# Kernel tuning notes

Hardware: AMD Instinct MI355X
Metric: run time of the kernel (lower is better)

Reference implementation:

```python
import jax, jax.numpy as jnp
import numpy as np

N_CLASSES = 2  # FS-MOL binary labels


def setup_inputs() -> dict:
    key = jax.random.key(0)
    k1, k2, k3 = jax.random.split(key, 3)
    Ns, Nq, d = 512, 16384, 512
    support_features = jax.random.normal(k1, (Ns, d), dtype=jnp.float32)
    support_labels = jax.random.randint(k2, (Ns,), 0, N_CLASSES, dtype=jnp.int64)
    query_features = jax.random.normal(k3, (Nq, d), dtype=jnp.float32)
    return {
        "support_features": support_features,
        "support_labels": support_labels,
        "query_features": query_features,
    }


def _cov(x):
    # rowvar=False covariance of [N, d] -> [d, d], matching _estimate_cov
    xc = x - jnp.mean(x, axis=0, keepdims=True)
    return (xc.T @ xc) / (x.shape[0] - 1)


def reference(support_features, support_labels, query_features):
    d = support_features.shape[1]
    dt = support_features.dtype
    task_cov = _cov(support_features)          # [d, d]
    reg = jnp.asarray(0.1, dt) * jnp.eye(d, dtype=dt)

    def per_class(c):
        mask = (support_labels == c).astype(dt)            # [Ns]
        n = mask.sum()                                      # scalar count
        mean = (mask[:, None] * support_features).sum(0) / n
        xc = (support_features - mean) * mask[:, None]      # zero out other classes
        cov_c = (xc.T @ xc) / (n - 1.0)
        lam = jnp.minimum(n / (n + 1.0), jnp.asarray(0.1, dt))
        prec = jnp.linalg.inv(lam * cov_c + (1.0 - lam) * task_cov + reg)
        return mean, prec

    means, precs = jax.vmap(per_class)(jnp.arange(N_CLASSES))  # [C,d], [C,d,d]

    # Mahalanobis: diff[c,q,:] = mean_c - query_q  (matches repeated_class_means - repeated_target)
    diff = means[:, None, :] - query_features[None, :, :]      # [C, Nq, d]
    h = jnp.einsum('cqd,cde->cqe', diff, precs)                # [C, Nq, d]
    logits = -(h * diff).sum(-1).T                             # [Nq, C]
    return logits
```

## Files before the change

### kernel.cpp

```cpp
#include <hip/hip_runtime.h>

#define NS 512
#define DF 512
#define NQ 16384

#define WS_MEAN0 0
#define WS_MEAN1 512
#define WS_MEANA 1024
#define WS_CNT   1536
#define WS_V0    2048
#define WS_V1    2560
#define WS_KC    3072
#define WS_M     4096
#define WS_PB    (WS_M + 2*DF*DF)
#define WS_QB    (WS_PB + DF*DF)
#define WS_GP    WS_QB

typedef __attribute__((ext_vector_type(8))) short short8;
typedef __attribute__((ext_vector_type(4))) float floatx4;

__device__ __forceinline__ unsigned short f2bf(float f) {
    unsigned u = __float_as_uint(f);
    unsigned r = (u + 0x7fffu + ((u >> 16) & 1u)) >> 16;
    return (unsigned short)r;
}

__device__ __forceinline__ float readlane_f(float v, int lane) {
    return __uint_as_float(__builtin_amdgcn_readlane(__float_as_uint(v), lane));
}

__device__ __forceinline__ void load_lds16(const void* g, void* l) {
    __builtin_amdgcn_global_load_lds(
        (const __attribute__((address_space(1))) unsigned int*)g,
        (__attribute__((address_space(3))) unsigned int*)l, 16, 0, 0);
}

__global__ __launch_bounds__(512) void k_stats(const float* __restrict__ S,
                                               const int* __restrict__ lab,
                                               float* __restrict__ ws) {
    __shared__ int lb[NS];
    __shared__ float r0[8][64], r1[8][64];
    __shared__ int rc[8];
    int tid = threadIdx.x;
    for (int l = tid; l < NS; l += 512) lb[l] = lab[l];
    __syncthreads();
    int dl = tid & 63, ch = tid >> 6;
    int dd = blockIdx.x * 64 + dl;
    float s0 = 0.f, s1 = 0.f;
    int n1 = 0;
    for (int n = ch * 64; n < ch * 64 + 64; ++n) {
        float v = S[n * DF + dd];
        if (lb[n]) { s1 += v; n1++; } else { s0 += v; }
    }
    r0[ch][dl] = s0; r1[ch][dl] = s1;
    if (dl == 0) rc[ch] = n1;
    __syncthreads();
    if (ch == 0) {
        float t0 = 0.f, t1 = 0.f; int n1t = 0;
#pragma unroll
        for (int x = 0; x < 8; ++x) { t0 += r0[x][dl]; t1 += r1[x][dl]; n1t += rc[x]; }
        float fn1 = (float)n1t, fn0 = (float)(NS - n1t);
        ws[WS_MEAN0 + dd] = t0 / fn0;
        ws[WS_MEAN1 + dd] = t1 / fn1;
        ws[WS_MEANA + dd] = (t0 + t1) / (float)NS;
        if (blockIdx.x == 0 && dl == 0) {
            ws[WS_CNT] = fn0; ws[WS_CNT + 1] = fn1;
            ws[WS_KC] = 0.f; ws[WS_KC + 1] = 0.f;
        }
    }
}

__global__ __launch_bounds__(256) void k_gram_part(const float* __restrict__ S,
                                                   const int* __restrict__ lab,
                                                   float* __restrict__ ws) {
    __shared__ float SA[16 * 65];
    __shared__ float SB[16 * 65];
    __shared__ int lb[16];
    int tx = threadIdx.x, ty = threadIdx.y;
    int tid = ty * 16 + tx;
    int i0 = blockIdx.x * 64, j0 = blockIdx.y * 64;
    int z = blockIdx.z;
    float a0[4][4] = {{0.f}}, a1[4][4] = {{0.f}};
    for (int nc = z * 64; nc < z * 64 + 64; nc += 16) {
#pragma unroll
        for (int l = 0; l < 4; ++l) {
            int idx = tid + 256 * l;
            int nn = idx >> 6, col = idx & 63;
            SA[nn * 65 + col] = S[(nc + nn) * DF + i0 + col];
            SB[nn * 65 + col] = S[(nc + nn) * DF + j0 + col];
        }
        if (tid < 16) lb[tid] = lab[nc + tid];
        __syncthreads();
#pragma unroll
        for (int kk = 0; kk < 16; ++kk) {
            float av[4], bv[4];
#pragma unroll
            for (int r = 0; r < 4; ++r) av[r] = SA[kk * 65 + ty * 4 + r];
#pragma unroll
            for (int s = 0; s < 4; ++s) bv[s] = SB[kk * 65 + tx * 4 + s];
            if (lb[kk]) {
#pragma unroll
                for (int r = 0; r < 4; ++r)
#pragma unroll
                    for (int s = 0; s < 4; ++s) a1[r][s] += av[r] * bv[s];
            } else {
#pragma unroll
                for (int r = 0; r < 4; ++r)
#pragma unroll
                    for (int s = 0; s < 4; ++s) a0[r][s] += av[r] * bv[s];
            }
        }
        __syncthreads();
    }
    float* Gp = ws + WS_GP;
#pragma unroll
    for (int r = 0; r < 4; ++r) {
        int i = i0 + ty * 4 + r;
#pragma unroll
        for (int s = 0; s < 4; ++s) {
            int j = j0 + tx * 4 + s;
            Gp[((z * 2 + 0) * DF + i) * DF + j] = a0[r][s];
            Gp[((z * 2 + 1) * DF + i) * DF + j] = a1[r][s];
        }
    }
}

__global__ __launch_bounds__(256) void k_asm(float* __restrict__ ws) {
    const float* Gp = ws + WS_GP;
    int e = blockIdx.x * 256 + threadIdx.x;
    int i = e >> 9, j = e & 511;
    float g0 = 0.f, g1 = 0.f;
#pragma unroll
    for (int ch = 0; ch < 8; ++ch) {
        g0 += Gp[((ch * 2 + 0) * DF + i) * DF + j];
        g1 += Gp[((ch * 2 + 1) * DF + i) * DF + j];
    }
    float n0 = ws[WS_CNT], n1 = ws[WS_CNT + 1];
    float lam0 = fminf(n0 / (n0 + 1.f), 0.1f);
    float lam1 = fminf(n1 / (n1 + 1.f), 0.1f);
    float m0i = ws[WS_MEAN0 + i], m1i = ws[WS_MEAN1 + i], mai = ws[WS_MEANA + i];
    float m0j = ws[WS_MEAN0 + j], m1j = ws[WS_MEAN1 + j], maj = ws[WS_MEANA + j];
    float task = (g0 + g1 - (float)NS * mai * maj) / (float)(NS - 1);
    float cov0 = (g0 - n0 * m0i * m0j) / (n0 - 1.f);
    float cov1 = (g1 - n1 * m1i * m1j) / (n1 - 1.f);
    float dg = (i == j) ? 0.1f : 0.f;
    ws[WS_M + i * DF + j] = lam0 * cov0 + (1.f - lam0) * task + dg;
    ws[WS_M + DF * DF + i * DF + j] = lam1 * cov1 + (1.f - lam1) * task + dg;
}

__global__ __launch_bounds__(256) void k_step(float* __restrict__ ws, int k, int wbf) {
    int c = blockIdx.y;
    int jh = blockIdx.z;
    int ti = blockIdx.x >> 3, tj = blockIdx.x & 7;
    float* Mb = ws + WS_M + c * DF * DF;
    float* Akk = Mb + (k * 64) * DF + k * 64;
    unsigned short* pb = (unsigned short*)(ws + WS_PB) + (size_t)c * DF * DF;
    __shared__ float T[64 * 65];
    __shared__ float LV[64 * 65];
    __shared__ float LU[64 * 33];
    __shared__ float D1[64 * 33];
    __shared__ float rbuf[2][4][64];
    int tid = threadIdx.x;
    int jl = tid & 63, w = tid >> 6;
    bool isdiag = (ti == k) && (tj == k);
    bool isrow = (ti == k) && (tj != k);
    bool iscol = (tj == k) && (ti != k);

#pragma unroll
    for (int m = 0; m < 16; ++m) {
        int idx = tid + 256 * m;
        int i = idx >> 6, j = idx & 63;
        T[i * 65 + j] = Akk[i * DF + j];
    }
    if (ti != k) {
        const float* src = Mb + (ti * 64) * DF + k * 64;
#pragma unroll
        for (int m = 0; m < 16; ++m) {
            int idx = tid + 256 * m;
            int i = idx >> 6, j = idx & 63;
            LV[i * 65 + j] = src[i * DF + j];
        }
    }
    if (tj != k) {
        const float* src = Mb + (k * 64) * DF + tj * 64 + jh * 32;
#pragma unroll
        for (int m = 0; m < 8; ++m) {
            int idx = tid + 256 * m;
            int i = idx >> 5, j = idx & 31;
            LU[i * 33 + j] = src[i * DF + j];
        }
    }
    __syncthreads();

    float Tr[16];
#pragma unroll
    for (int m = 0; m < 16; ++m) Tr[m] = T[(w * 16 + m) * 65 + jl];
#pragma unroll
    for (int r = 0; r < 16; ++r) {
        const int q0 = r * 4;
        const int par = r & 1;
        if (w == (q0 >> 4)) {
            const int mb = q0 & 15;
            rbuf[par][0][jl] = Tr[mb + 0];
            rbuf[par][1][jl] = Tr[mb + 1];
            rbuf[par][2][jl] = Tr[mb + 2];
            rbuf[par][3][jl] = Tr[mb + 3];
        }
        __syncthreads();
        float B[4][4];
#pragma unroll
        for (int a = 0; a < 4; ++a)
#pragma unroll
            for (int b = 0; b < 4; ++b) B[a][b] = rbuf[par][a][q0 + b];
#pragma unroll
        for (int p = 0; p < 4; ++p) {
            float piv = 1.0f / B[p][p];
#pragma unroll
            for (int j = 0; j < 4; ++j) if (j != p) B[p][j] *= piv;
#pragma unroll
            for (int i = 0; i < 4; ++i) if (i != p) {
                float f = B[i][p];
#pragma unroll
                for (int j = 0; j < 4; ++j) if (j != p) B[i][j] -= f * B[p][j];
                B[i][p] = -f * piv;
            }
            B[p][p] = piv;
        }
        float r0v = rbuf[par][0][jl], r1v = rbuf[par][1][jl];
        float r2v = rbuf[par][2][jl], r3v = rbuf[par][3][jl];
        float nr[4];
#pragma unroll
        for (int a = 0; a < 4; ++a)
            nr[a] = B[a][0] * r0v + B[a][1] * r1v + B[a][2] * r2v + B[a][3] * r3v;
        bool colin = ((jl >> 2) == r);
        int bsel = jl & 3;
        float Bc[4];
#pragma unroll
        for (int a = 0; a < 4; ++a)
            Bc[a] = bsel == 0 ? B[a][0]
                  : (bsel == 1 ? B[a][1] : (bsel == 2 ? B[a][2] : B[a][3]));
#pragma unroll
        for (int m = 0; m < 16; ++m) {
            float cv0 = readlane_f(Tr[m], q0 + 0);
            float cv1 = readlane_f(Tr[m], q0 + 1);
            float cv2 = readlane_f(Tr[m], q0 + 2);
            float cv3 = readlane_f(Tr[m], q0 + 3);
            float g = Tr[m] - (cv0 * nr[0] + cv1 * nr[1] + cv2 * nr[2] + cv3 * nr[3]);
            bool rowin = (((w * 16 + m) >> 2) == r);
            float gcol = -(cv0 * Bc[0] + cv1 * Bc[1] + cv2 * Bc[2] + cv3 * Bc[3]);
            if (rowin) g = nr[m & 3];
            if (colin) g = rowin ? Bc[m & 3] : gcol;
            Tr[m] = g;
        }
    }
#pragma unroll
    for (int m = 0; m < 16; ++m) T[(w * 16 + m) * 65 + jl] = Tr[m];
    __syncthreads();

    int tx8 = tid & 7, ty32 = tid >> 3;
    int cb0 = jh * 32;
    if (isdiag) {
#pragma unroll
        for (int m = 0; m < 8; ++m) {
            int idx = tid + 256 * m;
            int i = idx >> 5, j = idx & 31;
            float v = T[i * 65 + cb0 + j];
            Akk[i * DF + cb0 + j] = v;
            if (wbf) pb[(size_t)(k * 64 + i) * DF + k * 64 + cb0 + j] = f2bf(v);
        }
    } else if (isrow) {
        float acc[2][4] = {{0.f}};
        for (int kk = 0; kk < 64; ++kk) {
            float av[2], bv[4];
#pragma unroll
            for (int r = 0; r < 2; ++r) av[r] = T[(ty32 * 2 + r) * 65 + kk];
#pragma unroll
            for (int s = 0; s < 4; ++s) bv[s] = LU[kk * 33 + tx8 * 4 + s];
#pragma unroll
            for (int r = 0; r < 2; ++r)
#pragma unroll
                for (int s = 0; s < 4; ++s) acc[r][s] += av[r] * bv[s];
        }
        float* dst = Mb + (k * 64) * DF + tj * 64 + cb0;
#pragma unroll
        for (int r = 0; r < 2; ++r)
#pragma unroll
            for (int s = 0; s < 4; ++s) {
                float v = acc[r][s];
                dst[(ty32 * 2 + r) * DF + tx8 * 4 + s] = v;
                if (wbf) pb[(size_t)(k * 64 + ty32 * 2 + r) * DF + tj * 64 + cb0 + tx8 * 4 + s] = f2bf(v);
            }
    } else if (iscol) {
        float acc[2][4] = {{0.f}};
        for (int kk = 0; kk < 64; ++kk) {
            float av[2], bv[4];
#pragma unroll
            for (int r = 0; r < 2; ++r) av[r] = LV[(ty32 * 2 + r) * 65 + kk];
#pragma unroll
            for (int s = 0; s < 4; ++s) bv[s] = T[kk * 65 + cb0 + tx8 * 4 + s];
#pragma unroll
            for (int r = 0; r < 2; ++r)
#pragma unroll
                for (int s = 0; s < 4; ++s) acc[r][s] += av[r] * bv[s];
        }
        float* dst = Mb + (ti * 64) * DF + k * 64 + cb0;
#pragma unroll
        for (int r = 0; r < 2; ++r)
#pragma unroll
            for (int s = 0; s < 4; ++s) {
                float v = -acc[r][s];
                dst[(ty32 * 2 + r) * DF + tx8 * 4 + s] = v;
                if (wbf) pb[(size_t)(ti * 64 + ty32 * 2 + r) * DF + k * 64 + cb0 + tx8 * 4 + s] = f2bf(v);
            }
    } else {
        float a1[2][4] = {{0.f}};
        for (int kk = 0; kk < 64; ++kk) {
            float av[2], bv[4];
#pragma unroll
            for (int r = 0; r < 2; ++r) av[r] = T[(ty32 * 2 + r) * 65 + kk];
#pragma unroll
            for (int s = 0; s < 4; ++s) bv[s] = LU[kk * 33 + tx8 * 4 + s];
#pragma unroll
            for (int r = 0; r < 2; ++r)
#pragma unroll
                for (int s = 0; s < 4; ++s) a1[r][s] += av[r] * bv[s];
        }
        __syncthreads();
#pragma unroll
        for (int r = 0; r < 2; ++r)
#pragma unroll
            for (int s = 0; s < 4; ++s) D1[(ty32 * 2 + r) * 33 + tx8 * 4 + s] = a1[r][s];
        __syncthreads();
        float a2[2][4] = {{0.f}};
        for (int kk = 0; kk < 64; ++kk) {
            float av[2], bv[4];
#pragma unroll
            for (int r = 0; r < 2; ++r) av[r] = LV[(ty32 * 2 + r) * 65 + kk];
#pragma unroll
            for (int s = 0; s < 4; ++s) bv[s] = D1[kk * 33 + tx8 * 4 + s];
#pragma unroll
            for (int r = 0; r < 2; ++r)
#pragma unroll
                for (int s = 0; s < 4; ++s) a2[r][s] += av[r] * bv[s];
        }
        float* dst = Mb + (ti * 64) * DF + tj * 64 + cb0;
#pragma unroll
        for (int r = 0; r < 2; ++r)
#pragma unroll
            for (int s = 0; s < 4; ++s) {
                int off = (ty32 * 2 + r) * DF + tx8 * 4 + s;
                float nv = dst[off] - a2[r][s];
                dst[off] = nv;
                if (wbf) pb[(size_t)(ti * 64 + ty32 * 2 + r) * DF + tj * 64 + cb0 + tx8 * 4 + s] = f2bf(nv);
            }
    }
}

__global__ __launch_bounds__(256) void k_vk(float* __restrict__ ws) {
    int c = blockIdx.x >> 3, rb = blockIdx.x & 7;
    const float* P = ws + WS_M + c * DF * DF;
    const float* mc = ws + (c ? WS_MEAN1 : WS_MEAN0);
    float* v = ws + (c ? WS_V1 : WS_V0);
    __shared__ float ml[DF];
    __shared__ float red[4][64];
    int tid = threadIdx.x;
    for (int l = tid; l < DF; l += 256) ml[l] = mc[l];
    __syncthreads();
    int rl = tid & 63, ch = tid >> 6;
    int row = rb * 64 + rl;
    float dot = 0.f;
    const float* pr = P + (size_t)row * DF + ch * 128;
    for (int t = 0; t < 32; ++t) {
        float4 pv = *(const float4*)(pr + t * 4);
        const float* mm = ml + ch * 128 + t * 4;
        dot += pv.x * mm[0] + pv.y * mm[1] + pv.z * mm[2] + pv.w * mm[3];
    }
    red[ch][rl] = dot;
    __syncthreads();
    if (ch == 0) {
        float d = red[0][rl] + red[1][rl] + red[2][rl] + red[3][rl];
        v[row] = d;
        float kp = d * ml[row];
#pragma unroll
        for (int off = 32; off > 0; off >>= 1) kp += __shfl_down(kp, off);
        if (rl == 0) atomicAdd(&ws[WS_KC + c], kp);
    }
}

__global__ __launch_bounds__(256) void k_qinit(const float* __restrict__ Q,
                                               float* __restrict__ ws,
                                               float* __restrict__ out) {
    unsigned short* qbw = (unsigned short*)(ws + WS_QB);
    const float* v0 = ws + WS_V0;
    const float* v1 = ws + WS_V1;
    int lane = threadIdx.x & 63;
    int q = blockIdx.x * 4 + (threadIdx.x >> 6);
    const float* qrow = Q + (size_t)q * DF + lane * 8;
    float4 x0 = *(const float4*)(qrow);
    float4 x1 = *(const float4*)(qrow + 4);
    const float* v0p = v0 + lane * 8;
    const float* v1p = v1 + lane * 8;
    float4 w00 = *(const float4*)(v0p), w01 = *(const float4*)(v0p + 4);
    float4 w10 = *(const float4*)(v1p), w11 = *(const float4*)(v1p + 4);
    float a0 = x0.x * w00.x + x0.y * w00.y + x0.z * w00.z + x0.w * w00.w
             + x1.x * w01.x + x1.y * w01.y + x1.z * w01.z + x1.w * w01.w;
    float a1 = x0.x * w10.x + x0.y * w10.y + x0.z * w10.z + x0.w * w10.w
             + x1.x * w11.x + x1.y * w11.y + x1.z * w11.z + x1.w * w11.w;
    short8 r;
    r[0] = (short)f2bf(x0.x); r[1] = (short)f2bf(x0.y);
    r[2] = (short)f2bf(x0.z); r[3] = (short)f2bf(x0.w);
    r[4] = (short)f2bf(x1.x); r[5] = (short)f2bf(x1.y);
    r[6] = (short)f2bf(x1.z); r[7] = (short)f2bf(x1.w);
    *(short8*)(qbw + (size_t)q * DF + lane * 8) = r;
#pragma unroll
    for (int off = 32; off > 0; off >>= 1) {
        a0 += __shfl_down(a0, off);
        a1 += __shfl_down(a1, off);
    }
    if (lane == 0) {
        out[q * 2 + 0] = 2.f * a0 - ws[WS_KC + 0];
        out[q * 2 + 1] = 2.f * a1 - ws[WS_KC + 1];
    }
}

__global__ __launch_bounds__(256, 3) void k_gemm(const float* __restrict__ ws,
                                                 float* __restrict__ out) {
    const unsigned short* qb = (const unsigned short*)(ws + WS_QB);
    int c = blockIdx.y >> 2;
    int n0 = (blockIdx.y & 3) * 128;
    const unsigned short* pbc = (const unsigned short*)(ws + WS_PB) + (size_t)c * DF * DF;
    int q0 = blockIdx.x * 128;
    __shared__ __align__(16) unsigned short Abuf[128 * 64];
    __shared__ __align__(16) unsigned short Bbuf[128 * 64];
    int tid = threadIdx.x;
    int w = tid >> 6, lane = tid & 63;
    int quad = lane >> 4, l15 = lane & 15;
    floatx4 acc[2][8];
#pragma unroll
    for (int mt = 0; mt < 2; ++mt)
#pragma unroll
        for (int nt = 0; nt < 8; ++nt) acc[mt][nt] = (floatx4)(0.f);

    for (int kt = 0; kt < 8; ++kt) {
        int kc = kt * 64;
#pragma unroll
        for (int i = 0; i < 4; ++i) {
            int o = tid * 16 + i * 4096;
            int row = o >> 7;
            int sg = ((o >> 4) & 7) ^ (row & 7);
            load_lds16(qb + (size_t)(q0 + row) * DF + kc + sg * 8, (char*)Abuf + o);
        }
#pragma unroll
        for (int i = 0; i < 4; ++i) {
            int o = tid * 16 + i * 4096;
            int row = o >> 7;
            int sg = ((o >> 4) & 7) ^ (row & 7);
            load_lds16(pbc + (size_t)(n0 + row) * DF + kc + sg * 8, (char*)Bbuf + o);
        }
        __syncthreads();
#pragma unroll
        for (int kk2 = 0; kk2 < 2; ++kk2) {
            int u = ((kk2 * 4 + quad) ^ (l15 & 7)) << 4;
            short8 b[8];
#pragma unroll
            for (int nt = 0; nt < 8; ++nt)
                b[nt] = *(const short8*)((const char*)Bbuf + (nt * 16 + l15) * 128 + u);
#pragma unroll
            for (int mt = 0; mt < 2; ++mt) {
                short8 a = *(const short8*)((const char*)Abuf + (w * 32 + mt * 16 + l15) * 128 + u);
#pragma unroll
                for (int nt = 0; nt < 8; ++nt)
                    acc[mt][nt] = __builtin_amdgcn_mfma_f32_16x16x32_bf16(a, b[nt], acc[mt][nt], 0, 0, 0);
            }
        }
        __syncthreads();
    }
#pragma unroll
    for (int mt = 0; mt < 2; ++mt)
#pragma unroll
        for (int reg = 0; reg < 4; ++reg) {
            int row = w * 32 + mt * 16 + quad * 4 + reg;
            float part = 0.f;
#pragma unroll
            for (int nt = 0; nt < 8; ++nt) {
                float h = acc[mt][nt][reg];
                unsigned qu = qb[(size_t)(q0 + row) * DF + n0 + nt * 16 + l15];
                part += h * __uint_as_float(qu << 16);
            }
            part += __shfl_xor(part, 1);
            part += __shfl_xor(part, 2);
            part += __shfl_xor(part, 4);
            part += __shfl_xor(part, 8);
            if (l15 == 0) atomicAdd(&out[(size_t)(q0 + row) * 2 + c], -part);
        }
}

extern "C" void kernel_launch(void* const* d_in, const int* in_sizes, int n_in,
                              void* d_out, int out_size, void* d_ws, size_t ws_size,
                              hipStream_t stream) {
    const float* S = (const float*)d_in[0];
    const int* lab = (const int*)d_in[1];
    const float* Q = (const float*)d_in[2];
    float* out = (float*)d_out;
    float* ws = (float*)d_ws;

    k_stats<<<8, 512, 0, stream>>>(S, lab, ws);
    k_gram_part<<<dim3(8, 8, 8), dim3(16, 16), 0, stream>>>(S, lab, ws);
    k_asm<<<1024, 256, 0, stream>>>(ws);
    for (int k = 0; k < 8; ++k)
        k_step<<<dim3(64, 2, 2), 256, 0, stream>>>(ws, k, k == 7 ? 1 : 0);
    k_vk<<<16, 256, 0, stream>>>(ws);
    k_qinit<<<NQ / 4, 256, 0, stream>>>(Q, ws, out);
    k_gemm<<<dim3(NQ / 128, 8), 256, 0, stream>>>(ws, out);
}
```

Before: 393.9 us.

## Fuse covariance, block Gauss-Jordan inversion and mean-projection into one cooperative kernel

Replaces the separate stats, partial-Gram, assembly, eight Gauss-Jordan step and mean-projection launches with a single cooperative kernel of 256 blocks. Phases are separated by grid-wide syncs and share a union of LDS layouts. The aim is to remove per-launch overhead and the gaps between many small dependent kernels. In exchange, each block does more serial work (two Gram jobs, double-length stats loops), grid.sync adds its own barrier cost, and the kernel depends on all 256 blocks being co-resident.

Result: slower. 662.8 us (+68.3%).

```diff
diff --git a/kernel.cpp b/kernel.cpp
--- a/kernel.cpp
+++ b/kernel.cpp
@@ -1,4 +1,7 @@
 #include <hip/hip_runtime.h>
+#include <hip/hip_cooperative_groups.h>
+
+namespace cg = cooperative_groups;
 
 #define NS 512
 #define DF 512
@@ -35,355 +38,366 @@
         (__attribute__((address_space(3))) unsigned int*)l, 16, 0, 0);
 }
 
-__global__ __launch_bounds__(512) void k_stats(const float* __restrict__ S,
-                                               const int* __restrict__ lab,
-                                               float* __restrict__ ws) {
-    __shared__ int lb[NS];
-    __shared__ float r0[8][64], r1[8][64];
-    __shared__ int rc[8];
-    int tid = threadIdx.x;
-    for (int l = tid; l < NS; l += 512) lb[l] = lab[l];
-    __syncthreads();
-    int dl = tid & 63, ch = tid >> 6;
-    int dd = blockIdx.x * 64 + dl;
-    float s0 = 0.f, s1 = 0.f;
-    int n1 = 0;
-    for (int n = ch * 64; n < ch * 64 + 64; ++n) {
-        float v = S[n * DF + dd];
-        if (lb[n]) { s1 += v; n1++; } else { s0 += v; }
-    }
-    r0[ch][dl] = s0; r1[ch][dl] = s1;
-    if (dl == 0) rc[ch] = n1;
-    __syncthreads();
-    if (ch == 0) {
-        float t0 = 0.f, t1 = 0.f; int n1t = 0;
-#pragma unroll
-        for (int x = 0; x < 8; ++x) { t0 += r0[x][dl]; t1 += r1[x][dl]; n1t += rc[x]; }
-        float fn1 = (float)n1t, fn0 = (float)(NS - n1t);
-        ws[WS_MEAN0 + dd] = t0 / fn0;
-        ws[WS_MEAN1 + dd] = t1 / fn1;
-        ws[WS_MEANA + dd] = (t0 + t1) / (float)NS;
-        if (blockIdx.x == 0 && dl == 0) {
-            ws[WS_CNT] = fn0; ws[WS_CNT + 1] = fn1;
-            ws[WS_KC] = 0.f; ws[WS_KC + 1] = 0.f;
-        }
-    }
-}
-
-__global__ __launch_bounds__(256) void k_gram_part(const float* __restrict__ S,
-                                                   const int* __restrict__ lab,
-                                                   float* __restrict__ ws) {
-    __shared__ float SA[16 * 65];
-    __shared__ float SB[16 * 65];
-    __shared__ int lb[16];
-    int tx = threadIdx.x, ty = threadIdx.y;
-    int tid = ty * 16 + tx;
-    int i0 = blockIdx.x * 64, j0 = blockIdx.y * 64;
-    int z = blockIdx.z;
-    float a0[4][4] = {{0.f}}, a1[4][4] = {{0.f}};
-    for (int nc = z * 64; nc < z * 64 + 64; nc += 16) {
-#pragma unroll
-        for (int l = 0; l < 4; ++l) {
-            int idx = tid + 256 * l;
-            int nn = idx >> 6, col = idx & 63;
-            SA[nn * 65 + col] = S[(nc + nn) * DF + i0 + col];
-            SB[nn * 65 + col] = S[(nc + nn) * DF + j0 + col];
-        }
-        if (tid < 16) lb[tid] = lab[nc + tid];
-        __syncthreads();
-#pragma unroll
-        for (int kk = 0; kk < 16; ++kk) {
-            float av[4], bv[4];
-#pragma unroll
-            for (int r = 0; r < 4; ++r) av[r] = SA[kk * 65 + ty * 4 + r];
-#pragma unroll
-            for (int s = 0; s < 4; ++s) bv[s] = SB[kk * 65 + tx * 4 + s];
-            if (lb[kk]) {
-#pragma unroll
-                for (int r = 0; r < 4; ++r)
-#pragma unroll
-                    for (int s = 0; s < 4; ++s) a1[r][s] += av[r] * bv[s];
+struct SGram { float SA[16 * 65]; float SB[16 * 65]; int lb[16]; };
+struct SStats { int lb[NS]; float r0[4][64]; float r1[4][64]; int rc[4]; };
+struct SGJ { float T[64 * 65]; float LV[64 * 65]; float LU[64 * 33]; float D1[64 * 33]; float rbuf[2][4][64]; };
+struct SVk { float ml[DF]; float red[4][64]; };
+union SMem { SGram gr; SStats st; SGJ gj; SVk vk; };
+
+__global__ __launch_bounds__(256) void k_mega(const float* __restrict__ S,
+                                              const int* __restrict__ lab,
+                                              float* __restrict__ ws) {
+    cg::grid_group grid = cg::this_grid();
+    __shared__ SMem sm;
+    const int b = blockIdx.x;
+    const int tid = threadIdx.x;
+
+    if (b < 8) {
+        for (int l = tid; l < NS; l += 256) sm.st.lb[l] = lab[l];
+        __syncthreads();
+        int dl = tid & 63, ch = tid >> 6;
+        int dd = b * 64 + dl;
+        float s0 = 0.f, s1 = 0.f;
+        int n1 = 0;
+        for (int n = ch * 128; n < ch * 128 + 128; ++n) {
+            float v = S[n * DF + dd];
+            if (sm.st.lb[n]) { s1 += v; n1++; } else { s0 += v; }
+        }
+        sm.st.r0[ch][dl] = s0; sm.st.r1[ch][dl] = s1;
+        if (dl == 0) sm.st.rc[ch] = n1;
+        __syncthreads();
+        if (ch == 0) {
+            float t0 = 0.f, t1 = 0.f; int n1t = 0;
+#pragma unroll
+            for (int x = 0; x < 4; ++x) { t0 += sm.st.r0[x][dl]; t1 += sm.st.r1[x][dl]; n1t += sm.st.rc[x]; }
+            float fn1 = (float)n1t, fn0 = (float)(NS - n1t);
+            ws[WS_MEAN0 + dd] = t0 / fn0;
+            ws[WS_MEAN1 + dd] = t1 / fn1;
+            ws[WS_MEANA + dd] = (t0 + t1) / (float)NS;
+            if (b == 0 && dl == 0) {
+                ws[WS_CNT] = fn0; ws[WS_CNT + 1] = fn1;
+                ws[WS_KC] = 0.f; ws[WS_KC + 1] = 0.f;
+            }
+        }
+        __syncthreads();
+    }
+
+    {
+        int tx = tid & 15, ty = tid >> 4;
+        float* Gp = ws + WS_GP;
+        for (int jj = 0; jj < 2; ++jj) {
+            int job = b + jj * 256;
+            int i0 = (job & 7) * 64, j0 = ((job >> 3) & 7) * 64, z = job >> 6;
+            float a0[4][4] = {{0.f}}, a1[4][4] = {{0.f}};
+            for (int nc = z * 64; nc < z * 64 + 64; nc += 16) {
+#pragma unroll
+                for (int l = 0; l < 4; ++l) {
+                    int idx = tid + 256 * l;
+                    int nn = idx >> 6, col = idx & 63;
+                    sm.gr.SA[nn * 65 + col] = S[(nc + nn) * DF + i0 + col];
+                    sm.gr.SB[nn * 65 + col] = S[(nc + nn) * DF + j0 + col];
+                }
+                if (tid < 16) sm.gr.lb[tid] = lab[nc + tid];
+                __syncthreads();
+#pragma unroll
+                for (int kk = 0; kk < 16; ++kk) {
+                    float av[4], bv[4];
+#pragma unroll
+                    for (int r = 0; r < 4; ++r) av[r] = sm.gr.SA[kk * 65 + ty * 4 + r];
+#pragma unroll
+                    for (int s = 0; s < 4; ++s) bv[s] = sm.gr.SB[kk * 65 + tx * 4 + s];
+                    if (sm.gr.lb[kk]) {
+#pragma unroll
+                        for (int r = 0; r < 4; ++r)
+#pragma unroll
+                            for (int s = 0; s < 4; ++s) a1[r][s] += av[r] * bv[s];
+                    } else {
+#pragma unroll
+                        for (int r = 0; r < 4; ++r)
+#pragma unroll
+                            for (int s = 0; s < 4; ++s) a0[r][s] += av[r] * bv[s];
+                    }
+                }
+                __syncthreads();
+            }
+#pragma unroll
+            for (int r = 0; r < 4; ++r) {
+                int i = i0 + ty * 4 + r;
+#pragma unroll
+                for (int s = 0; s < 4; ++s) {
+                    int j = j0 + tx * 4 + s;
+                    Gp[((z * 2 + 0) * DF + i) * DF + j] = a0[r][s];
+                    Gp[((z * 2 + 1) * DF + i) * DF + j] = a1[r][s];
+                }
+            }
+        }
+    }
+    grid.sync();
+
+    {
+        const float* Gp = ws + WS_GP;
+        float n0 = ws[WS_CNT], n1 = ws[WS_CNT + 1];
+        float lam0 = fminf(n0 / (n0 + 1.f), 0.1f);
+        float lam1 = fminf(n1 / (n1 + 1.f), 0.1f);
+#pragma unroll
+        for (int u = 0; u < 4; ++u) {
+            int e = (b * 4 + u) * 256 + tid;
+            int i = e >> 9, j = e & 511;
+            float g0 = 0.f, g1 = 0.f;
+#pragma unroll
+            for (int ch = 0; ch < 8; ++ch) {
+                g0 += Gp[((ch * 2 + 0) * DF + i) * DF + j];
+                g1 += Gp[((ch * 2 + 1) * DF + i) * DF + j];
+            }
+            float m0i = ws[WS_MEAN0 + i], m1i = ws[WS_MEAN1 + i], mai = ws[WS_MEANA + i];
+            float m0j = ws[WS_MEAN0 + j], m1j = ws[WS_MEAN1 + j], maj = ws[WS_MEANA + j];
+            float task = (g0 + g1 - (float)NS * mai * maj) / (float)(NS - 1);
+            float cov0 = (g0 - n0 * m0i * m0j) / (n0 - 1.f);
+            float cov1 = (g1 - n1 * m1i * m1j) / (n1 - 1.f);
+            float dg = (i == j) ? 0.1f : 0.f;
+            ws[WS_M + i * DF + j] = lam0 * cov0 + (1.f - lam0) * task + dg;
+            ws[WS_M + DF * DF + i * DF + j] = lam1 * cov1 + (1.f - lam1) * task + dg;
+        }
+    }
+    grid.sync();
+
+    {
+        const int c = (b >> 6) & 1;
+        const int jh = b >> 7;
+        const int ti = (b & 63) >> 3, tj = b & 7;
+        float* Mb = ws + WS_M + c * DF * DF;
+        unsigned short* pb = (unsigned short*)(ws + WS_PB) + (size_t)c * DF * DF;
+        const int jl = tid & 63, w = tid >> 6;
+
+        for (int k = 0; k < 8; ++k) {
+            const int wbf = (k == 7) ? 1 : 0;
+            float* Akk = Mb + (k * 64) * DF + k * 64;
+            bool isdiag = (ti == k) && (tj == k);
+            bool isrow = (ti == k) && (tj != k);
+            bool iscol = (tj == k) && (ti != k);
+
+#pragma unroll
+            for (int m = 0; m < 16; ++m) {
+                int idx = tid + 256 * m;
+                int i = idx >> 6, j = idx & 63;
+                sm.gj.T[i * 65 + j] = Akk[i * DF + j];
+            }
+            if (ti != k) {
+                const float* src = Mb + (ti * 64) * DF + k * 64;
+#pragma unroll
+                for (int m = 0; m < 16; ++m) {
+                    int idx = tid + 256 * m;
+                    int i = idx >> 6, j = idx & 63;
+                    sm.gj.LV[i * 65 + j] = src[i * DF + j];
+                }
+            }
+            if (tj != k) {
+                const float* src = Mb + (k * 64) * DF + tj * 64 + jh * 32;
+#pragma unroll
+                for (int m = 0; m < 8; ++m) {
+                    int idx = tid + 256 * m;
+                    int i = idx >> 5, j = idx & 31;
+                    sm.gj.LU[i * 33 + j] = src[i * DF + j];
+                }
+            }
+            __syncthreads();
+
+            float Tr[16];
+#pragma unroll
+            for (int m = 0; m < 16; ++m) Tr[m] = sm.gj.T[(w * 16 + m) * 65 + jl];
+#pragma unroll
+            for (int r = 0; r < 16; ++r) {
+                const int q0 = r * 4;
+                const int par = r & 1;
+                if (w == (q0 >> 4)) {
+                    const int mb = q0 & 15;
+                    sm.gj.rbuf[par][0][jl] = Tr[mb + 0];
+                    sm.gj.rbuf[par][1][jl] = Tr[mb + 1];
+                    sm.gj.rbuf[par][2][jl] = Tr[mb + 2];
+                    sm.gj.rbuf[par][3][jl] = Tr[mb + 3];
+                }
+                __syncthreads();
+                float B[4][4];
+#pragma unroll
+                for (int a = 0; a < 4; ++a)
+#pragma unroll
+                    for (int bb = 0; bb < 4; ++bb) B[a][bb] = sm.gj.rbuf[par][a][q0 + bb];
+#pragma unroll
+                for (int p = 0; p < 4; ++p) {
+                    float piv = 1.0f / B[p][p];
+#pragma unroll
+                    for (int j = 0; j < 4; ++j) if (j != p) B[p][j] *= piv;
+#pragma unroll
+                    for (int i = 0; i < 4; ++i) if (i != p) {
+                        float f = B[i][p];
+#pragma unroll
+                        for (int j = 0; j < 4; ++j) if (j != p) B[i][j] -= f * B[p][j];
+                        B[i][p] = -f * piv;
+                    }
+                    B[p][p] = piv;
+                }
+                float r0v = sm.gj.rbuf[par][0][jl], r1v = sm.gj.rbuf[par][1][jl];
+                float r2v = sm.gj.rbuf[par][2][jl], r3v = sm.gj.rbuf[par][3][jl];
+                float nr[4];
+#pragma unroll
+                for (int a = 0; a < 4; ++a)
+                    nr[a] = B[a][0] * r0v + B[a][1] * r1v + B[a][2] * r2v + B[a][3] * r3v;
+                bool colin = ((jl >> 2) == r);
+                int bsel = jl & 3;
+                float Bc[4];
+#pragma unroll
+                for (int a = 0; a < 4; ++a)
+                    Bc[a] = bsel == 0 ? B[a][0]
+                          : (bsel == 1 ? B[a][1] : (bsel == 2 ? B[a][2] : B[a][3]));
+#pragma unroll
+                for (int m = 0; m < 16; ++m) {
+                    float cv0 = readlane_f(Tr[m], q0 + 0);
+                    float cv1 = readlane_f(Tr[m], q0 + 1);
+                    float cv2 = readlane_f(Tr[m], q0 + 2);
+                    float cv3 = readlane_f(Tr[m], q0 + 3);
+                    float g = Tr[m] - (cv0 * nr[0] + cv1 * nr[1] + cv2 * nr[2] + cv3 * nr[3]);
+                    bool rowin = (((w * 16 + m) >> 2) == r);
+                    float gcol = -(cv0 * Bc[0] + cv1 * Bc[1] + cv2 * Bc[2] + cv3 * Bc[3]);
+                    if (rowin) g = nr[m & 3];
+                    if (colin) g = rowin ? Bc[m & 3] : gcol;
+                    Tr[m] = g;
+                }
+            }
+#pragma unroll
+            for (int m = 0; m < 16; ++m) sm.gj.T[(w * 16 + m) * 65 + jl] = Tr[m];
+            __syncthreads();
+
+            int tx8 = tid & 7, ty32 = tid >> 3;
+            int cb0 = jh * 32;
+            if (isdiag) {
+#pragma unroll
+                for (int m = 0; m < 8; ++m) {
+                    int idx = tid + 256 * m;
+                    int i = idx >> 5, j = idx & 31;
+                    float v = sm.gj.T[i * 65 + cb0 + j];
+                    Akk[i * DF + cb0 + j] = v;
+                    if (wbf) pb[(size_t)(k * 64 + i) * DF + k * 64 + cb0 + j] = f2bf(v);
+                }
+            } else if (isrow) {
+                float acc[2][4] = {{0.f}};
+#pragma unroll 4
+                for (int kk = 0; kk < 64; ++kk) {
+                    float av[2], bv[4];
+#pragma unroll
+                    for (int r = 0; r < 2; ++r) av[r] = sm.gj.T[(ty32 * 2 + r) * 65 + kk];
+#pragma unroll
+                    for (int s = 0; s < 4; ++s) bv[s] = sm.gj.LU[kk * 33 + tx8 * 4 + s];
+#pragma unroll
+                    for (int r = 0; r < 2; ++r)
+#pragma unroll
+                        for (int s = 0; s < 4; ++s) acc[r][s] += av[r] * bv[s];
+                }
+                float* dst = Mb + (k * 64) * DF + tj * 64 + cb0;
+#pragma unroll
+                for (int r = 0; r < 2; ++r)
+#pragma unroll
+                    for (int s = 0; s < 4; ++s) {
+                        float v = acc[r][s];
+                        dst[(ty32 * 2 + r) * DF + tx8 * 4 + s] = v;
+                        if (wbf) pb[(size_t)(k * 64 + ty32 * 2 + r) * DF + tj * 64 + cb0 + tx8 * 4 + s] = f2bf(v);
+                    }
+            } else if (iscol) {
+                float acc[2][4] = {{0.f}};
+#pragma unroll 4
+                for (int kk = 0; kk < 64; ++kk) {
+                    float av[2], bv[4];
+#pragma unroll
+                    for (int r = 0; r < 2; ++r) av[r] = sm.gj.LV[(ty32 * 2 + r) * 65 + kk];
+#pragma unroll
+                    for (int s = 0; s < 4; ++s) bv[s] = sm.gj.T[kk * 65 + cb0 + tx8 * 4 + s];
+#pragma unroll
+                    for (int r = 0; r < 2; ++r)
+#pragma unroll
+                        for (int s = 0; s < 4; ++s) acc[r][s] += av[r] * bv[s];
+                }
+                float* dst = Mb + (ti * 64) * DF + k * 64 + cb0;
+#pragma unroll
+                for (int r = 0; r < 2; ++r)
+#pragma unroll
+                    for (int s = 0; s < 4; ++s) {
+                        float v = -acc[r][s];
+                        dst[(ty32 * 2 + r) * DF + tx8 * 4 + s] = v;
+                        if (wbf) pb[(size_t)(ti * 64 + ty32 * 2 + r) * DF + k * 64 + cb0 + tx8 * 4 + s] = f2bf(v);
+                    }
             } else {
-#pragma unroll
-                for (int r = 0; r < 4; ++r)
-#pragma unroll
-                    for (int s = 0; s < 4; ++s) a0[r][s] += av[r] * bv[s];
-            }
-        }
-        __syncthreads();
-    }
-    float* Gp = ws + WS_GP;
-#pragma unroll
-    for (int r = 0; r < 4; ++r) {
-        int i = i0 + ty * 4 + r;
-#pragma unroll
-        for (int s = 0; s < 4; ++s) {
-            int j = j0 + tx * 4 + s;
-            Gp[((z * 2 + 0) * DF + i) * DF + j] = a0[r][s];
-            Gp[((z * 2 + 1) * DF + i) * DF + j] = a1[r][s];
-        }
-    }
-}
-
-__global__ __launch_bounds__(256) void k_asm(float* __restrict__ ws) {
-    const float* Gp = ws + WS_GP;
-    int e = blockIdx.x * 256 + threadIdx.x;
-    int i = e >> 9, j = e & 511;
-    float g0 = 0.f, g1 = 0.f;
-#pragma unroll
-    for (int ch = 0; ch < 8; ++ch) {
-        g0 += Gp[((ch * 2 + 0) * DF + i) * DF + j];
-        g1 += Gp[((ch * 2 + 1) * DF + i) * DF + j];
-    }
-    float n0 = ws[WS_CNT], n1 = ws[WS_CNT + 1];
-    float lam0 = fminf(n0 / (n0 + 1.f), 0.1f);
-    float lam1 = fminf(n1 / (n1 + 1.f), 0.1f);
-    float m0i = ws[WS_MEAN0 + i], m1i = ws[WS_MEAN1 + i], mai = ws[WS_MEANA + i];
-    float m0j = ws[WS_MEAN0 + j], m1j = ws[WS_MEAN1 + j], maj = ws[WS_MEANA + j];
-    float task = (g0 + g1 - (float)NS * mai * maj) / (float)(NS - 1);
-    float cov0 = (g0 - n0 * m0i * m0j) / (n0 - 1.f);
-    float cov1 = (g1 - n1 * m1i * m1j) / (n1 - 1.f);
-    float dg = (i == j) ? 0.1f : 0.f;
-    ws[WS_M + i * DF + j] = lam0 * cov0 + (1.f - lam0) * task + dg;
-    ws[WS_M + DF * DF + i * DF + j] = lam1 * cov1 + (1.f - lam1) * task + dg;
-}
-
-__global__ __launch_bounds__(256) void k_step(float* __restrict__ ws, int k, int wbf) {
-    int c = blockIdx.y;
-    int jh = blockIdx.z;
-    int ti = blockIdx.x >> 3, tj = blockIdx.x & 7;
-    float* Mb = ws + WS_M + c * DF * DF;
-    float* Akk = Mb + (k * 64) * DF + k * 64;
-    unsigned short* pb = (unsigned short*)(ws + WS_PB) + (size_t)c * DF * DF;
-    __shared__ float T[64 * 65];
-    __shared__ float LV[64 * 65];
-    __shared__ float LU[64 * 33];
-    __shared__ float D1[64 * 33];
-    __shared__ float rbuf[2][4][64];
-    int tid = threadIdx.x;
-    int jl = tid & 63, w = tid >> 6;
-    bool isdiag = (ti == k) && (tj == k);
-    bool isrow = (ti == k) && (tj != k);
-    bool iscol = (tj == k) && (ti != k);
-
-#pragma unroll
-    for (int m = 0; m < 16; ++m) {
-        int idx = tid + 256 * m;
-        int i = idx >> 6, j = idx & 63;
-        T[i * 65 + j] = Akk[i * DF + j];
-    }
-    if (ti != k) {
-        const float* src = Mb + (ti * 64) * DF + k * 64;
-#pragma unroll
-        for (int m = 0; m < 16; ++m) {
-            int idx = tid + 256 * m;
-            int i = idx >> 6, j = idx & 63;
-            LV[i * 65 + j] = src[i * DF + j];
-        }
-    }
-    if (tj != k) {
-        const float* src = Mb + (k * 64) * DF + tj * 64 + jh * 32;
-#pragma unroll
-        for (int m = 0; m < 8; ++m) {
-            int idx = tid + 256 * m;
-            int i = idx >> 5, j = idx & 31;
-            LU[i * 33 + j] = src[i * DF + j];
-        }
-    }
-    __syncthreads();
-
-    float Tr[16];
-#pragma unroll
-    for (int m = 0; m < 16; ++m) Tr[m] = T[(w * 16 + m) * 65 + jl];
-#pragma unroll
-    for (int r = 0; r < 16; ++r) {
-        const int q0 = r * 4;
-        const int par = r & 1;
-        if (w == (q0 >> 4)) {
-            const int mb = q0 & 15;
-            rbuf[par][0][jl] = Tr[mb + 0];
-            rbuf[par][1][jl] = Tr[mb + 1];
-            rbuf[par][2][jl] = Tr[mb + 2];
-            rbuf[par][3][jl] = Tr[mb + 3];
-        }
-        __syncthreads();
-        float B[4][4];
-#pragma unroll
-        for (int a = 0; a < 4; ++a)
-#pragma unroll
-            for (int b = 0; b < 4; ++b) B[a][b] = rbuf[par][a][q0 + b];
-#pragma unroll
-        for (int p = 0; p < 4; ++p) {
-            float piv = 1.0f / B[p][p];
-#pragma unroll
-            for (int j = 0; j < 4; ++j) if (j != p) B[p][j] *= piv;
-#pragma unroll
-            for (int i = 0; i < 4; ++i) if (i != p) {
-                float f = B[i][p];
-#pragma unroll
-                for (int j = 0; j < 4; ++j) if (j != p) B[i][j] -= f * B[p][j];
-                B[i][p] = -f * piv;
-            }
-            B[p][p] = piv;
-        }
-        float r0v = rbuf[par][0][jl], r1v = rbuf[par][1][jl];
-        float r2v = rbuf[par][2][jl], r3v = rbuf[par][3][jl];
-        float nr[4];
-#pragma unroll
-        for (int a = 0; a < 4; ++a)
-            nr[a] = B[a][0] * r0v + B[a][1] * r1v + B[a][2] * r2v + B[a][3] * r3v;
-        bool colin = ((jl >> 2) == r);
-        int bsel = jl & 3;
-        float Bc[4];
-#pragma unroll
-        for (int a = 0; a < 4; ++a)
-            Bc[a] = bsel == 0 ? B[a][0]
-                  : (bsel == 1 ? B[a][1] : (bsel == 2 ? B[a][2] : B[a][3]));
-#pragma unroll
-        for (int m = 0; m < 16; ++m) {
-            float cv0 = readlane_f(Tr[m], q0 + 0);
-            float cv1 = readlane_f(Tr[m], q0 + 1);
-            float cv2 = readlane_f(Tr[m], q0 + 2);
-            float cv3 = readlane_f(Tr[m], q0 + 3);
-            float g = Tr[m] - (cv0 * nr[0] + cv1 * nr[1] + cv2 * nr[2] + cv3 * nr[3]);
-            bool rowin = (((w * 16 + m) >> 2) == r);
-            float gcol = -(cv0 * Bc[0] + cv1 * Bc[1] + cv2 * Bc[2] + cv3 * Bc[3]);
-            if (rowin) g = nr[m & 3];
-            if (colin) g = rowin ? Bc[m & 3] : gcol;
-            Tr[m] = g;
-        }
-    }
-#pragma unroll
-    for (int m = 0; m < 16; ++m) T[(w * 16 + m) * 65 + jl] = Tr[m];
-    __syncthreads();
-
-    int tx8 = tid & 7, ty32 = tid >> 3;
-    int cb0 = jh * 32;
-    if (isdiag) {
-#pragma unroll
-        for (int m = 0; m < 8; ++m) {
-            int idx = tid + 256 * m;
-            int i = idx >> 5, j = idx & 31;
-            float v = T[i * 65 + cb0 + j];
-            Akk[i * DF + cb0 + j] = v;
-            if (wbf) pb[(size_t)(k * 64 + i) * DF + k * 64 + cb0 + j] = f2bf(v);
-        }
-    } else if (isrow) {
-        float acc[2][4] = {{0.f}};
-        for (int kk = 0; kk < 64; ++kk) {
-            float av[2], bv[4];
-#pragma unroll
-            for (int r = 0; r < 2; ++r) av[r] = T[(ty32 * 2 + r) * 65 + kk];
-#pragma unroll
-            for (int s = 0; s < 4; ++s) bv[s] = LU[kk * 33 + tx8 * 4 + s];
-#pragma unroll
-            for (int r = 0; r < 2; ++r)
-#pragma unroll
-                for (int s = 0; s < 4; ++s) acc[r][s] += av[r] * bv[s];
-        }
-        float* dst = Mb + (k * 64) * DF + tj * 64 + cb0;
-#pragma unroll
-        for (int r = 0; r < 2; ++r)
-#pragma unroll
-            for (int s = 0; s < 4; ++s) {
-                float v = acc[r][s];
-                dst[(ty32 * 2 + r) * DF + tx8 * 4 + s] = v;
-                if (wbf) pb[(size_t)(k * 64 + ty32 * 2 + r) * DF + tj * 64 + cb0 + tx8 * 4 + s] = f2bf(v);
-            }
-    } else if (iscol) {
-        float acc[2][4] = {{0.f}};
-        for (int kk = 0; kk < 64; ++kk) {
-            float av[2], bv[4];
-#pragma unroll
-            for (int r = 0; r < 2; ++r) av[r] = LV[(ty32 * 2 + r) * 65 + kk];
-#pragma unroll
-            for (int s = 0; s < 4; ++s) bv[s] = T[kk * 65 + cb0 + tx8 * 4 + s];
-#pragma unroll
-            for (int r = 0; r < 2; ++r)
-#pragma unroll
-                for (int s = 0; s < 4; ++s) acc[r][s] += av[r] * bv[s];
-        }
-        float* dst = Mb + (ti * 64) * DF + k * 64 + cb0;
-#pragma unroll
-        for (int r = 0; r < 2; ++r)
-#pragma unroll
-            for (int s = 0; s < 4; ++s) {
-                float v = -acc[r][s];
-                dst[(ty32 * 2 + r) * DF + tx8 * 4 + s] = v;
-                if (wbf) pb[(size_t)(ti * 64 + ty32 * 2 + r) * DF + k * 64 + cb0 + tx8 * 4 + s] = f2bf(v);
-            }
-    } else {
-        float a1[2][4] = {{0.f}};
-        for (int kk = 0; kk < 64; ++kk) {
-            float av[2], bv[4];
-#pragma unroll
-            for (int r = 0; r < 2; ++r) av[r] = T[(ty32 * 2 + r) * 65 + kk];
-#pragma unroll
-            for (int s = 0; s < 4; ++s) bv[s] = LU[kk * 33 + tx8 * 4 + s];
-#pragma unroll
-            for (int r = 0; r < 2; ++r)
-#pragma unroll
-                for (int s = 0; s < 4; ++s) a1[r][s] += av[r] * bv[s];
-        }
-        __syncthreads();
-#pragma unroll
-        for (int r = 0; r < 2; ++r)
-#pragma unroll
-            for (int s = 0; s < 4; ++s) D1[(ty32 * 2 + r) * 33 + tx8 * 4 + s] = a1[r][s];
-        __syncthreads();
-        float a2[2][4] = {{0.f}};
-        for (int kk = 0; kk < 64; ++kk) {
-            float av[2], bv[4];
-#pragma unroll
-            for (int r = 0; r < 2; ++r) av[r] = LV[(ty32 * 2 + r) * 65 + kk];
-#pragma unroll
-            for (int s = 0; s < 4; ++s) bv[s] = D1[kk * 33 + tx8 * 4 + s];
-#pragma unroll
-            for (int r = 0; r < 2; ++r)
-#pragma unroll
-                for (int s = 0; s < 4; ++s) a2[r][s] += av[r] * bv[s];
-        }
-        float* dst = Mb + (ti * 64) * DF + tj * 64 + cb0;
-#pragma unroll
-        for (int r = 0; r < 2; ++r)
-#pragma unroll
-            for (int s = 0; s < 4; ++s) {
-                int off = (ty32 * 2 + r) * DF + tx8 * 4 + s;
-                float nv = dst[off] - a2[r][s];
-                dst[off] = nv;
-                if (wbf) pb[(size_t)(ti * 64 + ty32 * 2 + r) * DF + tj * 64 + cb0 + tx8 * 4 + s] = f2bf(nv);
-            }
-    }
-}
-
-__global__ __launch_bounds__(256) void k_vk(float* __restrict__ ws) {
-    int c = blockIdx.x >> 3, rb = blockIdx.x & 7;
-    const float* P = ws + WS_M + c * DF * DF;
-    const float* mc = ws + (c ? WS_MEAN1 : WS_MEAN0);
-    float* v = ws + (c ? WS_V1 : WS_V0);
-    __shared__ float ml[DF];
-    __shared__ float red[4][64];
-    int tid = threadIdx.x;
-    for (int l = tid; l < DF; l += 256) ml[l] = mc[l];
-    __syncthreads();
-    int rl = tid & 63, ch = tid >> 6;
-    int row = rb * 64 + rl;
-    float dot = 0.f;
-    const float* pr = P + (size_t)row * DF + ch * 128;
-    for (int t = 0; t < 32; ++t) {
-        float4 pv = *(const float4*)(pr + t * 4);
-        const float* mm = ml + ch * 128 + t * 4;
-        dot += pv.x * mm[0] + pv.y * mm[1] + pv.z * mm[2] + pv.w * mm[3];
-    }
-    red[ch][rl] = dot;
-    __syncthreads();
-    if (ch == 0) {
-        float d = red[0][rl] + red[1][rl] + red[2][rl] + red[3][rl];
-        v[row] = d;
-        float kp = d * ml[row];
-#pragma unroll
-        for (int off = 32; off > 0; off >>= 1) kp += __shfl_down(kp, off);
-        if (rl == 0) atomicAdd(&ws[WS_KC + c], kp);
+                float a1[2][4] = {{0.f}};
+#pragma unroll 4
+                for (int kk = 0; kk < 64; ++kk) {
+                    float av[2], bv[4];
+#pragma unroll
+                    for (int r = 0; r < 2; ++r) av[r] = sm.gj.T[(ty32 * 2 + r) * 65 + kk];
+#pragma unroll
+                    for (int s = 0; s < 4; ++s) bv[s] = sm.gj.LU[kk * 33 + tx8 * 4 + s];
+#pragma unroll
+                    for (int r = 0; r < 2; ++r)
+#pragma unroll
+                        for (int s = 0; s < 4; ++s) a1[r][s] += av[r] * bv[s];
+                }
+                __syncthreads();
+#pragma unroll
+                for (int r = 0; r < 2; ++r)
+#pragma unroll
+                    for (int s = 0; s < 4; ++s) sm.gj.D1[(ty32 * 2 + r) * 33 + tx8 * 4 + s] = a1[r][s];
+                __syncthreads();
+                float a2[2][4] = {{0.f}};
+#pragma unroll 4
+                for (int kk = 0; kk < 64; ++kk) {
+                    float av[2], bv[4];
+#pragma unroll
+                    for (int r = 0; r < 2; ++r) av[r] = sm.gj.LV[(ty32 * 2 + r) * 65 + kk];
+#pragma unroll
+                    for (int s = 0; s < 4; ++s) bv[s] = sm.gj.D1[kk * 33 + tx8 * 4 + s];
+#pragma unroll
+                    for (int r = 0; r < 2; ++r)
+#pragma unroll
+                        for (int s = 0; s < 4; ++s) a2[r][s] += av[r] * bv[s];
+                }
+                float* dst = Mb + (ti * 64) * DF + tj * 64 + cb0;
+#pragma unroll
+                for (int r = 0; r < 2; ++r)
+#pragma unroll
+                    for (int s = 0; s < 4; ++s) {
+                        int off = (ty32 * 2 + r) * DF + tx8 * 4 + s;
+                        float nv = dst[off] - a2[r][s];
+                        dst[off] = nv;
+                        if (wbf) pb[(size_t)(ti * 64 + ty32 * 2 + r) * DF + tj * 64 + cb0 + tx8 * 4 + s] = f2bf(nv);
+                    }
+            }
+            grid.sync();
+        }
+    }
+
+    if (b < 16) {
+        int c = b >> 3, rb = b & 7;
+        const float* P = ws + WS_M + c * DF * DF;
+        const float* mc = ws + (c ? WS_MEAN1 : WS_MEAN0);
+        float* v = ws + (c ? WS_V1 : WS_V0);
+        for (int l = tid; l < DF; l += 256) sm.vk.ml[l] = mc[l];
+        __syncthreads();
+        int rl = tid & 63, ch = tid >> 6;
+        int row = rb * 64 + rl;
+        float dot = 0.f;
+        const float* pr = P + (size_t)row * DF + ch * 128;
+        for (int t = 0; t < 32; ++t) {
+            float4 pv = *(const float4*)(pr + t * 4);
+            const float* mm = sm.vk.ml + ch * 128 + t * 4;
+            dot += pv.x * mm[0] + pv.y * mm[1] + pv.z * mm[2] + pv.w * mm[3];
+        }
+        sm.vk.red[ch][rl] = dot;
+        __syncthreads();
+        if (ch == 0) {
+            float d = sm.vk.red[0][rl] + sm.vk.red[1][rl] + sm.vk.red[2][rl] + sm.vk.red[3][rl];
+            v[row] = d;
+            float kp = d * sm.vk.ml[row];
+#pragma unroll
+            for (int off = 32; off > 0; off >>= 1) kp += __shfl_down(kp, off);
+            if (rl == 0) atomicAdd(&ws[WS_KC + c], kp);
+        }
     }
 }
 
@@ -461,16 +475,16 @@
 #pragma unroll
         for (int kk2 = 0; kk2 < 2; ++kk2) {
             int u = ((kk2 * 4 + quad) ^ (l15 & 7)) << 4;
-            short8 b[8];
+            short8 bfrag[8];
 #pragma unroll
             for (int nt = 0; nt < 8; ++nt)
-                b[nt] = *(const short8*)((const char*)Bbuf + (nt * 16 + l15) * 128 + u);
+                bfrag[nt] = *(const short8*)((const char*)Bbuf + (nt * 16 + l15) * 128 + u);
 #pragma unroll
             for (int mt = 0; mt < 2; ++mt) {
                 short8 a = *(const short8*)((const char*)Abuf + (w * 32 + mt * 16 + l15) * 128 + u);
 #pragma unroll
                 for (int nt = 0; nt < 8; ++nt)
-                    acc[mt][nt] = __builtin_amdgcn_mfma_f32_16x16x32_bf16(a, b[nt], acc[mt][nt], 0, 0, 0);
+                    acc[mt][nt] = __builtin_amdgcn_mfma_f32_16x16x32_bf16(a, bfrag[nt], acc[mt][nt], 0, 0, 0);
             }
         }
         __syncthreads();
@@ -504,12 +518,8 @@
     float* out = (float*)d_out;
     float* ws = (float*)d_ws;
 
-    k_stats<<<8, 512, 0, stream>>>(S, lab, ws);
-    k_gram_part<<<dim3(8, 8, 8), dim3(16, 16), 0, stream>>>(S, lab, ws);
-    k_asm<<<1024, 256, 0, stream>>>(ws);
-    for (int k = 0; k < 8; ++k)
-        k_step<<<dim3(64, 2, 2), 256, 0, stream>>>(ws, k, k == 7 ? 1 : 0);
-    k_vk<<<16, 256, 0, stream>>>(ws);
+    void* args[3] = {(void*)&S, (void*)&lab, (void*)&ws};
+    hipLaunchCooperativeKernel((void*)k_mega, dim3(256), dim3(256), args, 0, stream);
     k_qinit<<<NQ / 4, 256, 0, stream>>>(Q, ws, out);
     k_gemm<<<dim3(NQ / 128, 8), 256, 0, stream>>>(ws, out);
 }
```
